# Kernel tuning notes

Hardware: AMD Instinct MI355X
Metric: run time of the kernel (lower is better)

## Reference

```python
import jax, jax.numpy as jnp
import numpy as np

D_MODEL = 2048
N_EXPERTS = 8
LOSS_SCALE = 3e-06


def setup_inputs() -> dict:
    key = jax.random.key(0)
    k_x, k_wr, k_br, k_w, k_b = jax.random.split(key, 5)
    s = 1.0 / np.sqrt(D_MODEL)
    x = jax.random.normal(k_x, (4, 2048, D_MODEL), dtype=jnp.float32)
    # router: nn.Linear(D, E) -> weight (E, D), bias (E,)
    Wr = jax.random.uniform(k_wr, (N_EXPERTS, D_MODEL), dtype=jnp.float32, minval=-s, maxval=s)
    br = jax.random.uniform(k_br, (N_EXPERTS,), dtype=jnp.float32, minval=-s, maxval=s)
    # experts: E stacked nn.Linear(D, D) -> weight (E, D_out, D_in), bias (E, D)
    W = jax.random.uniform(k_w, (N_EXPERTS, D_MODEL, D_MODEL), dtype=jnp.float32, minval=-s, maxval=s)
    b = jax.random.uniform(k_b, (N_EXPERTS, D_MODEL), dtype=jnp.float32, minval=-s, maxval=s)
    return {"x": x, "Wr": Wr, "br": br, "W": W, "b": b}


def reference(x, Wr, br, W, b):
    B, S, D = x.shape
    E = Wr.shape[0]
    xt = x.reshape(B * S, D)          # (T, D)
    T = xt.shape[0]

    logits = xt @ Wr.T + br           # (T, E)
    probs = jax.nn.softmax(logits, axis=-1)
    idx = jnp.argmax(probs, axis=-1)  # top-1 expert per token
    topp = jnp.max(probs, axis=-1)    # gating weight
    onehot = jax.nn.one_hot(idx, E, dtype=xt.dtype)  # (T, E)

    # auxiliary load-balancing loss (matches torch compute_loss exactly)
    fractions = onehot.mean(axis=0)                              # (E,)
    probability = (onehot * topp[:, None]).sum(axis=0) / (T * T)  # (E,)
    loss = jnp.sum(fractions * probability) * LOSS_SCALE * E

    # all-expert outputs then top-1 select (dense grouped GEMM form)
    y_all = jnp.einsum('td,efd->tef', xt, W) + b[None, :, :]     # (T, E, D)
    y = jnp.einsum('tef,te->tf', y_all, onehot) * topp[:, None]  # (T, D)
    return y.reshape(B, S, D), loss
```

## Files before the change

### kernel.cpp

```cpp
#include <hip/hip_runtime.h>

typedef unsigned short u16;
typedef unsigned int u32;
typedef __attribute__((ext_vector_type(8))) __bf16 bf16x8;
typedef __attribute__((ext_vector_type(4))) float f32x4;

#define T_TOK 8192
#define DMODEL 2048
#define N_EXP 8
#define NT 32

__device__ __forceinline__ u32 f2bf_bits(float f) {
    u32 u = __builtin_bit_cast(u32, f);
    return (u + 0x7fffu + ((u >> 16) & 1u)) >> 16;
}
__device__ __forceinline__ u32 pack2(float a, float b) {
    return f2bf_bits(a) | (f2bf_bits(b) << 16);
}

__device__ __forceinline__ void load_lds16(const u16* g, u16* l) {
    void* gnc = (void*)g;
    __builtin_amdgcn_global_load_lds(
        (__attribute__((address_space(1))) void*)gnc,
        (__attribute__((address_space(3))) void*)l,
        16, 0, 0);
}

__global__ void zero_kernel(u32* p) {
    p[threadIdx.x] = 0u;
}

__global__ void __launch_bounds__(256) prep_kernel(const float* __restrict__ x,
                                                   const float* __restrict__ Wr,
                                                   const float* __restrict__ br,
                                                   const float* __restrict__ W,
                                                   u16* __restrict__ Wb,
                                                   u16* __restrict__ xb,
                                                   int* __restrict__ perm,
                                                   float* __restrict__ topp,
                                                   int* __restrict__ counts,
                                                   float* __restrict__ sumt) {
    __shared__ int sEid[16];
    __shared__ float sTp[16];

    int bx = blockIdx.x;
    int tid = threadIdx.x;

    if (bx >= 512) {
        size_t i = ((size_t)(bx - 512) * 256 + tid) * 8;
        float4 a = *(const float4*)(W + i);
        float4 c = *(const float4*)(W + i + 4);
        uint4 o;
        o.x = pack2(a.x, a.y);
        o.y = pack2(a.z, a.w);
        o.z = pack2(c.x, c.y);
        o.w = pack2(c.z, c.w);
        *(uint4*)(Wb + i) = o;
        return;
    }

    int lane = tid & 63;
    int w = tid >> 6;
    int t0 = bx * 16 + w * 4;

    float acc[4][8];
#pragma unroll
    for (int tk = 0; tk < 4; tk++)
#pragma unroll
        for (int e = 0; e < 8; e++) acc[tk][e] = 0.0f;

#pragma unroll
    for (int i = 0; i < 8; i++) {
        int vidx = i * 64 + lane;
        float4 wv[8];
#pragma unroll
        for (int e = 0; e < 8; e++)
            wv[e] = *(const float4*)(Wr + e * DMODEL + vidx * 4);
#pragma unroll
        for (int tk = 0; tk < 4; tk++) {
            int t = t0 + tk;
            float4 xv = ((const float4*)(x + ((size_t)t << 11)))[vidx];
            uint2 pk;
            pk.x = pack2(xv.x, xv.y);
            pk.y = pack2(xv.z, xv.w);
            *(uint2*)(xb + ((size_t)t << 11) + (size_t)vidx * 4) = pk;
#pragma unroll
            for (int e = 0; e < 8; e++) {
                acc[tk][e] = fmaf(xv.x, wv[e].x, fmaf(xv.y, wv[e].y,
                              fmaf(xv.z, wv[e].z, fmaf(xv.w, wv[e].w, acc[tk][e]))));
            }
        }
    }
#pragma unroll
    for (int off = 32; off; off >>= 1)
#pragma unroll
        for (int tk = 0; tk < 4; tk++)
#pragma unroll
            for (int e = 0; e < 8; e++)
                acc[tk][e] += __shfl_xor(acc[tk][e], off, 64);

    if (lane == 0) {
#pragma unroll
        for (int tk = 0; tk < 4; tk++) {
            float lg[8];
#pragma unroll
            for (int e = 0; e < 8; e++) lg[e] = acc[tk][e] + br[e];
            float m = lg[0];
            int am = 0;
#pragma unroll
            for (int e = 1; e < 8; e++)
                if (lg[e] > m) { m = lg[e]; am = e; }
            float s = 0.0f;
#pragma unroll
            for (int e = 0; e < 8; e++) s += __expf(lg[e] - m);
            float tp = 1.0f / s;
            sEid[w * 4 + tk] = am;
            sTp[w * 4 + tk] = tp;
            topp[t0 + tk] = tp;
        }
    }
    __syncthreads();
    if (tid < 16) {
        int e = sEid[tid];
        float tp = sTp[tid];
        int pos = atomicAdd(&counts[e * 16], 1);
        perm[(e << 13) + pos] = bx * 16 + tid;
        atomicAdd(&sumt[e * 16], tp);
    }
}

__global__ void __launch_bounds__(512, 2) moe_gemm_kernel(const u16* __restrict__ xb,
                                                          const u16* __restrict__ Wb,
                                                          const float* __restrict__ bias,
                                                          const int* __restrict__ perm,
                                                          const int* __restrict__ counts,
                                                          const float* __restrict__ topp,
                                                          float* __restrict__ out) {
    __shared__ __align__(16) u16 lds[65536];

    int bid = blockIdx.x;
    int e  = bid & 7;
    int tc = (bid >> 3) & 7;
    int tr = bid >> 6;
    int cnt = counts[e * 16];
    int row0 = tr << 8;
    if (row0 >= cnt) return;
    int n0 = tc << 8;

    int tid = threadIdx.x;
    int lane = tid & 63;
    int wid = tid >> 6;
    int wr = wid >> 2;
    int wc = wid & 3;

    const int* permE = perm + (e << 13);
    const u16* WbE = Wb + ((size_t)e << 22);

    const u16* gA[4];
    const u16* gB[4];
    int sOff[4];
#pragma unroll
    for (int j = 0; j < 4; j++) {
        int s = tid + j * 512;
        int r = s >> 3;
        int cg = (s & 7) ^ (r & 7);
        int ta = permE[min(row0 + r, cnt - 1)];
        gA[j] = xb + ((size_t)ta << 11) + (cg << 3);
        gB[j] = WbE + ((size_t)(n0 + r) << 11) + (cg << 3);
        sOff[j] = s * 8;
    }

#define STG_A(QB, J, KO) load_lds16(gA[J] + (KO), lds + (QB) + sOff[J])
#define STG_B(QB, J, KO) load_lds16(gB[J] + (KO), lds + (QB) + 32768 + sOff[J])
#define VM4 asm volatile("s_waitcnt vmcnt(4)" ::: "memory")
#define VM2 asm volatile("s_waitcnt vmcnt(2)" ::: "memory")
#define VMN ((void)0)

    STG_A(0, 0, 0); STG_A(0, 2, 0);
    STG_B(0, 0, 0); STG_B(0, 1, 0);
    STG_B(0, 2, 0); STG_B(0, 3, 0);
    STG_A(0, 1, 0); STG_A(0, 3, 0);

    int mrow = lane & 15;
    int kq = lane >> 4;
    int s7 = mrow & 7;
    int mb = wr << 7;
    int nb = wc << 6;

    f32x4 acc[8][4];
#pragma unroll
    for (int mi = 0; mi < 8; mi++)
#pragma unroll
        for (int ni = 0; ni < 4; ni++)
            acc[mi][ni] = (f32x4){0.0f, 0.0f, 0.0f, 0.0f};

    VM2;
    asm volatile("s_barrier" ::: "memory");

#define PHASE(QB, MG, KS, S1, S2, VMW)                                         \
    {                                                                          \
        int kcs = ((KS) * 4 + kq) ^ s7;                                        \
        const u16* pa = lds + (QB) + ((mb + (MG) * 64 + mrow) * 8 + kcs) * 8;  \
        const u16* pb = lds + (QB) + 32768 + ((nb + mrow) * 8 + kcs) * 8;      \
        bf16x8 a0 = *(const bf16x8*)(pa);                                      \
        bf16x8 a1 = *(const bf16x8*)(pa + 1024);                               \
        bf16x8 a2 = *(const bf16x8*)(pa + 2048);                               \
        bf16x8 a3 = *(const bf16x8*)(pa + 3072);                               \
        bf16x8 b0 = *(const bf16x8*)(pb);                                      \
        bf16x8 b1 = *(const bf16x8*)(pb + 1024);                               \
        bf16x8 b2 = *(const bf16x8*)(pb + 2048);                               \
        bf16x8 b3 = *(const bf16x8*)(pb + 3072);                               \
        S1; S2;                                                                \
        asm volatile("s_barrier" ::: "memory");                                \
        __builtin_amdgcn_s_setprio(1);                                         \
        acc[(MG)*4+0][0] = __builtin_amdgcn_mfma_f32_16x16x32_bf16(a0, b0, acc[(MG)*4+0][0], 0, 0, 0); \
        acc[(MG)*4+0][1] = __builtin_amdgcn_mfma_f32_16x16x32_bf16(a0, b1, acc[(MG)*4+0][1], 0, 0, 0); \
        acc[(MG)*4+0][2] = __builtin_amdgcn_mfma_f32_16x16x32_bf16(a0, b2, acc[(MG)*4+0][2], 0, 0, 0); \
        acc[(MG)*4+0][3] = __builtin_amdgcn_mfma_f32_16x16x32_bf16(a0, b3, acc[(MG)*4+0][3], 0, 0, 0); \
        acc[(MG)*4+1][0] = __builtin_amdgcn_mfma_f32_16x16x32_bf16(a1, b0, acc[(MG)*4+1][0], 0, 0, 0); \
        acc[(MG)*4+1][1] = __builtin_amdgcn_mfma_f32_16x16x32_bf16(a1, b1, acc[(MG)*4+1][1], 0, 0, 0); \
        acc[(MG)*4+1][2] = __builtin_amdgcn_mfma_f32_16x16x32_bf16(a1, b2, acc[(MG)*4+1][2], 0, 0, 0); \
        acc[(MG)*4+1][3] = __builtin_amdgcn_mfma_f32_16x16x32_bf16(a1, b3, acc[(MG)*4+1][3], 0, 0, 0); \
        acc[(MG)*4+2][0] = __builtin_amdgcn_mfma_f32_16x16x32_bf16(a2, b0, acc[(MG)*4+2][0], 0, 0, 0); \
        acc[(MG)*4+2][1] = __builtin_amdgcn_mfma_f32_16x16x32_bf16(a2, b1, acc[(MG)*4+2][1], 0, 0, 0); \
        acc[(MG)*4+2][2] = __builtin_amdgcn_mfma_f32_16x16x32_bf16(a2, b2, acc[(MG)*4+2][2], 0, 0, 0); \
        acc[(MG)*4+2][3] = __builtin_amdgcn_mfma_f32_16x16x32_bf16(a2, b3, acc[(MG)*4+2][3], 0, 0, 0); \
        acc[(MG)*4+3][0] = __builtin_amdgcn_mfma_f32_16x16x32_bf16(a3, b0, acc[(MG)*4+3][0], 0, 0, 0); \
        acc[(MG)*4+3][1] = __builtin_amdgcn_mfma_f32_16x16x32_bf16(a3, b1, acc[(MG)*4+3][1], 0, 0, 0); \
        acc[(MG)*4+3][2] = __builtin_amdgcn_mfma_f32_16x16x32_bf16(a3, b2, acc[(MG)*4+3][2], 0, 0, 0); \
        acc[(MG)*4+3][3] = __builtin_amdgcn_mfma_f32_16x16x32_bf16(a3, b3, acc[(MG)*4+3][3], 0, 0, 0); \
        __builtin_amdgcn_s_setprio(0);                                         \
        VMW;                                                                   \
        asm volatile("s_barrier" ::: "memory");                                \
    }

#pragma unroll 1
    for (int t = 0; t < NT; t += 2) {
        int ko1 = (t + 1) << 6;
        int ko2 = (t + 2 < NT ? t + 2 : NT - 1) << 6;
        PHASE(0,     0, 0, STG_A(16384, 0, ko1), STG_A(16384, 2, ko1), VMN);
        PHASE(0,     0, 1, STG_B(16384, 0, ko1), STG_B(16384, 1, ko1), VM4);
        PHASE(0,     1, 0, STG_B(16384, 2, ko1), STG_B(16384, 3, ko1), VMN);
        PHASE(0,     1, 1, STG_A(16384, 1, ko1), STG_A(16384, 3, ko1), VM2);
        PHASE(16384, 0, 0, STG_A(0, 0, ko2), STG_A(0, 2, ko2), VMN);
        PHASE(16384, 0, 1, STG_B(0, 0, ko2), STG_B(0, 1, ko2), VM4);
        PHASE(16384, 1, 0, STG_B(0, 2, ko2), STG_B(0, 3, ko2), VMN);
        PHASE(16384, 1, 1, STG_A(0, 1, ko2), STG_A(0, 3, ko2), VM2);
    }

    const float* bE = bias + (e << 11);
    float bv[4];
#pragma unroll
    for (int ni = 0; ni < 4; ni++)
        bv[ni] = bE[n0 + nb + ni * 16 + mrow];

    int rb = row0 + mb + ((lane >> 4) << 2);
#pragma unroll
    for (int mi = 0; mi < 8; mi++) {
        int t_[4]; float tp_[4]; int v_[4];
#pragma unroll
        for (int r = 0; r < 4; r++) {
            int gr = rb + mi * 16 + r;
            v_[r] = gr < cnt;
            int grc = v_[r] ? gr : (cnt - 1);
            t_[r] = permE[grc];
            tp_[r] = topp[t_[r]];
        }
#pragma unroll
        for (int ni = 0; ni < 4; ni++) {
            int col = n0 + nb + ni * 16 + mrow;
            f32x4 v = acc[mi][ni];
#pragma unroll
            for (int r = 0; r < 4; r++) {
                if (v_[r])
                    out[((size_t)t_[r] << 11) + col] = (v[r] + bv[ni]) * tp_[r];
            }
        }
    }
}

__global__ void loss_kernel(const int* __restrict__ counts,
                            const float* __restrict__ sumt,
                            float* __restrict__ lossOut) {
    if (threadIdx.x == 0) {
        float acc = 0.0f;
        for (int e = 0; e < 8; e++) {
            float frac = (float)counts[e * 16] / 8192.0f;
            float prob = sumt[e * 16] / (8192.0f * 8192.0f);
            acc = fmaf(frac, prob, acc);
        }
        lossOut[0] = acc * 3e-6f * 8.0f;
    }
}

extern "C" void kernel_launch(void* const* d_in, const int* in_sizes, int n_in,
                              void* d_out, int out_size, void* d_ws, size_t ws_size,
                              hipStream_t stream) {
    const float* x  = (const float*)d_in[0];
    const float* Wr = (const float*)d_in[1];
    const float* br = (const float*)d_in[2];
    const float* W  = (const float*)d_in[3];
    const float* b  = (const float*)d_in[4];
    float* out = (float*)d_out;

    char* ws = (char*)d_ws;
    u16* Wb     = (u16*)ws;
    u16* xb     = (u16*)(ws + 67108864);
    int* perm   = (int*)(ws + 100663296);
    float* topp = (float*)(ws + 100925440);
    int* counts = (int*)(ws + 100958208);
    float* sumt = (float*)(ws + 100958720);

    zero_kernel<<<1, 256, 0, stream>>>((u32*)counts);
    prep_kernel<<<512 + 16384, 256, 0, stream>>>(x, Wr, br, W, Wb, xb, perm,
                                                 topp, counts, sumt);
    moe_gemm_kernel<<<N_EXP * 8 * 32, 512, 0, stream>>>(xb, Wb, b, perm, counts,
                                                        topp, out);
    loss_kernel<<<1, 64, 0, stream>>>(counts, sumt, out + (size_t)T_TOK * DMODEL);
}
```

Before: 404.0 us.

## Enlarge MoE GEMM row tile to 320 with reworked LDS staging schedule

The per-block M tile of the grouped expert GEMM grows from 256 to 320 token rows. Each wave now covers 160 rows through five A fragments per phase, and the LDS buffers are resized to hold the larger A tiles. Global-to-LDS staging is reordered so that B tiles, then A tiles, then the extra A slice are issued in separate phases, with matching vmcnt waits. The aim is to reuse each W tile across more tokens and launch fewer row tiles, at the cost of more accumulator registers, more LDS, and possibly more wasted padded rows in each expert's last tile.

```diff
diff --git a/kernel.cpp b/kernel.cpp
--- a/kernel.cpp
+++ b/kernel.cpp
@@ -9,6 +9,8 @@
 #define DMODEL 2048
 #define N_EXP 8
 #define NT 32
+#define MTILE 320
+#define MAX_TR 26
 
 __device__ __forceinline__ u32 f2bf_bits(float f) {
     u32 u = __builtin_bit_cast(u32, f);
@@ -136,14 +138,14 @@
                                                           const int* __restrict__ counts,
                                                           const float* __restrict__ topp,
                                                           float* __restrict__ out) {
-    __shared__ __align__(16) u16 lds[65536];
+    __shared__ __align__(16) u16 lds[73728];
 
     int bid = blockIdx.x;
     int e  = bid & 7;
     int tc = (bid >> 3) & 7;
     int tr = bid >> 6;
     int cnt = counts[e * 16];
-    int row0 = tr << 8;
+    int row0 = tr * MTILE;
     if (row0 >= cnt) return;
     int n0 = tc << 8;
 
@@ -156,81 +158,80 @@
     const int* permE = perm + (e << 13);
     const u16* WbE = Wb + ((size_t)e << 22);
 
-    const u16* gA[4];
+    const u16* gA[5];
     const u16* gB[4];
-    int sOff[4];
-#pragma unroll
-    for (int j = 0; j < 4; j++) {
+    int sOff[5];
+#pragma unroll
+    for (int j = 0; j < 5; j++) {
         int s = tid + j * 512;
         int r = s >> 3;
         int cg = (s & 7) ^ (r & 7);
         int ta = permE[min(row0 + r, cnt - 1)];
         gA[j] = xb + ((size_t)ta << 11) + (cg << 3);
-        gB[j] = WbE + ((size_t)(n0 + r) << 11) + (cg << 3);
+        if (j < 4) gB[j] = WbE + ((size_t)(n0 + r) << 11) + (cg << 3);
         sOff[j] = s * 8;
     }
 
-#define STG_A(QB, J, KO) load_lds16(gA[J] + (KO), lds + (QB) + sOff[J])
-#define STG_B(QB, J, KO) load_lds16(gB[J] + (KO), lds + (QB) + 32768 + sOff[J])
-#define VM4 asm volatile("s_waitcnt vmcnt(4)" ::: "memory")
-#define VM2 asm volatile("s_waitcnt vmcnt(2)" ::: "memory")
+#define STG_A(P, J, KO) load_lds16(gA[J] + (KO), lds + (P) * 20480 + sOff[J])
+#define STG_B(P, J, KO) load_lds16(gB[J] + (KO), lds + 40960 + (P) * 16384 + sOff[J])
+#define SB4(P, KO) { STG_B(P,0,KO); STG_B(P,1,KO); STG_B(P,2,KO); STG_B(P,3,KO); }
+#define SA4(P, KO) { STG_A(P,0,KO); STG_A(P,1,KO); STG_A(P,2,KO); STG_A(P,3,KO); }
+#define SA1(P, KO) { STG_A(P,4,KO); }
+#define VM8 asm volatile("s_waitcnt vmcnt(8)" ::: "memory")
+#define VM1 asm volatile("s_waitcnt vmcnt(1)" ::: "memory")
 #define VMN ((void)0)
-
-    STG_A(0, 0, 0); STG_A(0, 2, 0);
-    STG_B(0, 0, 0); STG_B(0, 1, 0);
-    STG_B(0, 2, 0); STG_B(0, 3, 0);
-    STG_A(0, 1, 0); STG_A(0, 3, 0);
 
     int mrow = lane & 15;
     int kq = lane >> 4;
     int s7 = mrow & 7;
-    int mb = wr << 7;
+    int mb = wr * 160;
     int nb = wc << 6;
 
-    f32x4 acc[8][4];
-#pragma unroll
-    for (int mi = 0; mi < 8; mi++)
-#pragma unroll
-        for (int ni = 0; ni < 4; ni++)
-            acc[mi][ni] = (f32x4){0.0f, 0.0f, 0.0f, 0.0f};
-
-    VM2;
+    f32x4 acc[2][5][4];
+#pragma unroll
+    for (int mg = 0; mg < 2; mg++)
+#pragma unroll
+        for (int i = 0; i < 5; i++)
+#pragma unroll
+            for (int ni = 0; ni < 4; ni++)
+                acc[mg][i][ni] = (f32x4){0.0f, 0.0f, 0.0f, 0.0f};
+
+    SB4(0, 0); SA4(0, 0); SA1(0, 0);
+    VM1;
     asm volatile("s_barrier" ::: "memory");
 
-#define PHASE(QB, MG, KS, S1, S2, VMW)                                         \
+#define MFMA4(MG, I, AV)                                                                     \
+    acc[MG][I][0] = __builtin_amdgcn_mfma_f32_16x16x32_bf16(AV, bv0, acc[MG][I][0], 0, 0, 0); \
+    acc[MG][I][1] = __builtin_amdgcn_mfma_f32_16x16x32_bf16(AV, bv1, acc[MG][I][1], 0, 0, 0); \
+    acc[MG][I][2] = __builtin_amdgcn_mfma_f32_16x16x32_bf16(AV, bv2, acc[MG][I][2], 0, 0, 0); \
+    acc[MG][I][3] = __builtin_amdgcn_mfma_f32_16x16x32_bf16(AV, bv3, acc[MG][I][3], 0, 0, 0);
+
+#define PH(PB, MG, KS, STMTS, WAIT)                                            \
     {                                                                          \
         int kcs = ((KS) * 4 + kq) ^ s7;                                        \
-        const u16* pa = lds + (QB) + ((mb + (MG) * 64 + mrow) * 8 + kcs) * 8;  \
-        const u16* pb = lds + (QB) + 32768 + ((nb + mrow) * 8 + kcs) * 8;      \
-        bf16x8 a0 = *(const bf16x8*)(pa);                                      \
-        bf16x8 a1 = *(const bf16x8*)(pa + 1024);                               \
-        bf16x8 a2 = *(const bf16x8*)(pa + 2048);                               \
-        bf16x8 a3 = *(const bf16x8*)(pa + 3072);                               \
-        bf16x8 b0 = *(const bf16x8*)(pb);                                      \
-        bf16x8 b1 = *(const bf16x8*)(pb + 1024);                               \
-        bf16x8 b2 = *(const bf16x8*)(pb + 2048);                               \
-        bf16x8 b3 = *(const bf16x8*)(pb + 3072);                               \
-        S1; S2;                                                                \
+        const u16* pa = lds + (PB) * 20480 +                                   \
+                        ((mb + (MG) * 80 + mrow) * 8 + kcs) * 8;               \
+        const u16* pb = lds + 40960 + (PB) * 16384 +                           \
+                        ((nb + mrow) * 8 + kcs) * 8;                           \
+        bf16x8 av0 = *(const bf16x8*)(pa);                                     \
+        bf16x8 av1 = *(const bf16x8*)(pa + 1024);                              \
+        bf16x8 av2 = *(const bf16x8*)(pa + 2048);                              \
+        bf16x8 av3 = *(const bf16x8*)(pa + 3072);                              \
+        bf16x8 av4 = *(const bf16x8*)(pa + 4096);                              \
+        bf16x8 bv0 = *(const bf16x8*)(pb);                                     \
+        bf16x8 bv1 = *(const bf16x8*)(pb + 1024);                              \
+        bf16x8 bv2 = *(const bf16x8*)(pb + 2048);                              \
+        bf16x8 bv3 = *(const bf16x8*)(pb + 3072);                              \
+        STMTS;                                                                 \
         asm volatile("s_barrier" ::: "memory");                                \
         __builtin_amdgcn_s_setprio(1);                                         \
-        acc[(MG)*4+0][0] = __builtin_amdgcn_mfma_f32_16x16x32_bf16(a0, b0, acc[(MG)*4+0][0], 0, 0, 0); \
-        acc[(MG)*4+0][1] = __builtin_amdgcn_mfma_f32_16x16x32_bf16(a0, b1, acc[(MG)*4+0][1], 0, 0, 0); \
-        acc[(MG)*4+0][2] = __builtin_amdgcn_mfma_f32_16x16x32_bf16(a0, b2, acc[(MG)*4+0][2], 0, 0, 0); \
-        acc[(MG)*4+0][3] = __builtin_amdgcn_mfma_f32_16x16x32_bf16(a0, b3, acc[(MG)*4+0][3], 0, 0, 0); \
-        acc[(MG)*4+1][0] = __builtin_amdgcn_mfma_f32_16x16x32_bf16(a1, b0, acc[(MG)*4+1][0], 0, 0, 0); \
-        acc[(MG)*4+1][1] = __builtin_amdgcn_mfma_f32_16x16x32_bf16(a1, b1, acc[(MG)*4+1][1], 0, 0, 0); \
-        acc[(MG)*4+1][2] = __builtin_amdgcn_mfma_f32_16x16x32_bf16(a1, b2, acc[(MG)*4+1][2], 0, 0, 0); \
-        acc[(MG)*4+1][3] = __builtin_amdgcn_mfma_f32_16x16x32_bf16(a1, b3, acc[(MG)*4+1][3], 0, 0, 0); \
-        acc[(MG)*4+2][0] = __builtin_amdgcn_mfma_f32_16x16x32_bf16(a2, b0, acc[(MG)*4+2][0], 0, 0, 0); \
-        acc[(MG)*4+2][1] = __builtin_amdgcn_mfma_f32_16x16x32_bf16(a2, b1, acc[(MG)*4+2][1], 0, 0, 0); \
-        acc[(MG)*4+2][2] = __builtin_amdgcn_mfma_f32_16x16x32_bf16(a2, b2, acc[(MG)*4+2][2], 0, 0, 0); \
-        acc[(MG)*4+2][3] = __builtin_amdgcn_mfma_f32_16x16x32_bf16(a2, b3, acc[(MG)*4+2][3], 0, 0, 0); \
-        acc[(MG)*4+3][0] = __builtin_amdgcn_mfma_f32_16x16x32_bf16(a3, b0, acc[(MG)*4+3][0], 0, 0, 0); \
-        acc[(MG)*4+3][1] = __builtin_amdgcn_mfma_f32_16x16x32_bf16(a3, b1, acc[(MG)*4+3][1], 0, 0, 0); \
-        acc[(MG)*4+3][2] = __builtin_amdgcn_mfma_f32_16x16x32_bf16(a3, b2, acc[(MG)*4+3][2], 0, 0, 0); \
-        acc[(MG)*4+3][3] = __builtin_amdgcn_mfma_f32_16x16x32_bf16(a3, b3, acc[(MG)*4+3][3], 0, 0, 0); \
+        MFMA4((MG), 0, av0)                                                    \
+        MFMA4((MG), 1, av1)                                                    \
+        MFMA4((MG), 2, av2)                                                    \
+        MFMA4((MG), 3, av3)                                                    \
+        MFMA4((MG), 4, av4)                                                    \
         __builtin_amdgcn_s_setprio(0);                                         \
-        VMW;                                                                   \
+        WAIT;                                                                  \
         asm volatile("s_barrier" ::: "memory");                                \
     }
 
@@ -238,45 +239,47 @@
     for (int t = 0; t < NT; t += 2) {
         int ko1 = (t + 1) << 6;
         int ko2 = (t + 2 < NT ? t + 2 : NT - 1) << 6;
-        PHASE(0,     0, 0, STG_A(16384, 0, ko1), STG_A(16384, 2, ko1), VMN);
-        PHASE(0,     0, 1, STG_B(16384, 0, ko1), STG_B(16384, 1, ko1), VM4);
-        PHASE(0,     1, 0, STG_B(16384, 2, ko1), STG_B(16384, 3, ko1), VMN);
-        PHASE(0,     1, 1, STG_A(16384, 1, ko1), STG_A(16384, 3, ko1), VM2);
-        PHASE(16384, 0, 0, STG_A(0, 0, ko2), STG_A(0, 2, ko2), VMN);
-        PHASE(16384, 0, 1, STG_B(0, 0, ko2), STG_B(0, 1, ko2), VM4);
-        PHASE(16384, 1, 0, STG_B(0, 2, ko2), STG_B(0, 3, ko2), VMN);
-        PHASE(16384, 1, 1, STG_A(0, 1, ko2), STG_A(0, 3, ko2), VM2);
+        PH(0, 0, 0, SB4(1, ko1), VMN);
+        PH(0, 0, 1, SA4(1, ko1), VM8);
+        PH(0, 1, 0, SA1(1, ko1), VMN);
+        PH(0, 1, 1, ;,           VM1);
+        PH(1, 0, 0, SB4(0, ko2), VMN);
+        PH(1, 0, 1, SA4(0, ko2), VM8);
+        PH(1, 1, 0, SA1(0, ko2), VMN);
+        PH(1, 1, 1, ;,           VM1);
     }
 
     const float* bE = bias + (e << 11);
-    float bv[4];
+    float bvx[4];
 #pragma unroll
     for (int ni = 0; ni < 4; ni++)
-        bv[ni] = bE[n0 + nb + ni * 16 + mrow];
-
-    int rb = row0 + mb + ((lane >> 4) << 2);
-#pragma unroll
-    for (int mi = 0; mi < 8; mi++) {
-        int t_[4]; float tp_[4]; int v_[4];
-#pragma unroll
-        for (int r = 0; r < 4; r++) {
-            int gr = rb + mi * 16 + r;
-            v_[r] = gr < cnt;
-            int grc = v_[r] ? gr : (cnt - 1);
-            t_[r] = permE[grc];
-            tp_[r] = topp[t_[r]];
-        }
-#pragma unroll
-        for (int ni = 0; ni < 4; ni++) {
-            int col = n0 + nb + ni * 16 + mrow;
-            f32x4 v = acc[mi][ni];
+        bvx[ni] = bE[n0 + nb + ni * 16 + mrow];
+
+#pragma unroll
+    for (int mg = 0; mg < 2; mg++)
+#pragma unroll
+        for (int i = 0; i < 5; i++) {
+            int rbase = row0 + mb + mg * 80 + i * 16 + ((lane >> 4) << 2);
+            int t_[4]; float tp_[4]; int v_[4];
 #pragma unroll
             for (int r = 0; r < 4; r++) {
-                if (v_[r])
-                    out[((size_t)t_[r] << 11) + col] = (v[r] + bv[ni]) * tp_[r];
+                int gr = rbase + r;
+                v_[r] = gr < cnt;
+                int grc = v_[r] ? gr : (cnt - 1);
+                t_[r] = permE[grc];
+                tp_[r] = topp[t_[r]];
+            }
+#pragma unroll
+            for (int ni = 0; ni < 4; ni++) {
+                int col = n0 + nb + ni * 16 + mrow;
+                f32x4 v = acc[mg][i][ni];
+#pragma unroll
+                for (int r = 0; r < 4; r++) {
+                    if (v_[r])
+                        out[((size_t)t_[r] << 11) + col] = (v[r] + bvx[ni]) * tp_[r];
+                }
             }
         }
-    }
 }
 
 __global__ void loss_kernel(const int* __restrict__ counts,
@@ -314,7 +317,7 @@
     zero_kernel<<<1, 256, 0, stream>>>((u32*)counts);
     prep_kernel<<<512 + 16384, 256, 0, stream>>>(x, Wr, br, W, Wb, xb, perm,
                                                  topp, counts, sumt);
-    moe_gemm_kernel<<<N_EXP * 8 * 32, 512, 0, stream>>>(xb, Wb, b, perm, counts,
-                                                        topp, out);
+    moe_gemm_kernel<<<N_EXP * 8 * MAX_TR, 512, 0, stream>>>(xb, Wb, b, perm,
+                                                            counts, topp, out);
     loss_kernel<<<1, 64, 0, stream>>>(counts, sumt, out + (size_t)T_TOK * DMODEL);
 }
```

After: 365.7 us. 9.5% less time.
